# Kernel optimization log

Measured on AMD Instinct MI355X. Metric: run time of the kernel, lower is better.

Reference implementation:

```python
import jax, jax.numpy as jnp
import numpy as np


def fps(p, m):
    """Furthest point sampling. p: (B,N,3) -> idx (B,m) int32. Starts at index 0 like pointops."""
    p = jax.lax.stop_gradient(p)
    B, N, _ = p.shape
    d2 = jnp.full((B, N), jnp.inf, dtype=p.dtype)  # min sq-dist to selected set
    first = jnp.zeros((B,), dtype=jnp.int32)

    def step(carry, _):
        d2, last = carry
        lastp = jnp.take_along_axis(p, last[:, None, None].astype(jnp.int32), axis=1)  # (B,1,3)
        dist = jnp.sum((p - lastp) ** 2, axis=-1)  # (B,N)
        d2 = jnp.minimum(d2, dist)
        nxt = jnp.argmax(d2, axis=-1).astype(jnp.int32)
        return (d2, nxt), last

    _, idx = jax.lax.scan(step, (d2, first), None, length=m)
    return jnp.transpose(idx)  # (B,m)


def knn_indices(p1, p2, k):
    """k nearest neighbors of p2 (B,M,3) among p1 (B,N,3) -> (B,M,k) int32."""
    p1 = jax.lax.stop_gradient(p1)
    p2 = jax.lax.stop_gradient(p2)
    # squared distances (B,M,N)
    d2 = (jnp.sum(p2 ** 2, -1)[:, :, None]
          + jnp.sum(p1 ** 2, -1)[:, None, :]
          - 2.0 * jnp.einsum('bmd,bnd->bmn', p2, p1))
    _, idx = jax.lax.top_k(-d2, k)
    return idx.astype(jnp.int32)


def setup_inputs() -> dict:
    key = jax.random.key(0)
    k1, k2 = jax.random.split(key)
    B, N, C = 8, 8192, 64
    p1 = jax.random.normal(k1, (B, N, 3), dtype=jnp.float32)
    x = jax.random.normal(k2, (B, N, C), dtype=jnp.float32)
    return {"p1": p1, "x": x, "stride": 4, "num_neighbors": 16}


def reference(p1, x, stride, num_neighbors):
    B, N, C = x.shape
    M = N // stride
    idx = fps(p1, M)                                   # (B,M) int32
    p2 = jnp.take_along_axis(p1, idx[:, :, None], 1)   # (B,M,3) sampled coords
    nn = knn_indices(p1, p2, num_neighbors)            # (B,M,k)
    # gather features: (B,M,k,C)
    grouped = jax.vmap(lambda xb, ib: xb[ib])(x, nn)
    y = jnp.mean(grouped, axis=2)                      # (B,M,C)
    return (y, p2, idx)
```

## Files before the change

kernel.cpp:

```cpp
#include <hip/hip_runtime.h>

#define Bn 8
#define Nn 8192
#define Cn 64
#define Mn 2048
#define Kn 16
#define FPS_T 512
#define CPT 16
#define NWAVE (FPS_T / 64)
#define NCELL 4096
#define CELLS_PT (NCELL / FPS_T)

typedef unsigned long long u64;
typedef unsigned u32;

__device__ __forceinline__ u64 u64max(u64 a, u64 b) { return a > b ? a : b; }

template <int CTRL, int RMASK>
__device__ __forceinline__ void dpp_kmax_step(u32& hi, u32& lo) {
    const u32 h2 = (u32)__builtin_amdgcn_update_dpp((int)hi, (int)hi, CTRL, RMASK, 0xF, false);
    const u32 l2 = (u32)__builtin_amdgcn_update_dpp((int)lo, (int)lo, CTRL, RMASK, 0xF, false);
    const u64 a = ((u64)hi << 32) | lo;
    const u64 bb = ((u64)h2 << 32) | l2;
    if (bb > a) { hi = h2; lo = l2; }
}
__device__ __forceinline__ void wave_kmax(u32& hi, u32& lo) {
    dpp_kmax_step<0x111, 0xF>(hi, lo);
    dpp_kmax_step<0x112, 0xF>(hi, lo);
    dpp_kmax_step<0x114, 0xF>(hi, lo);
    dpp_kmax_step<0x118, 0xF>(hi, lo);
    dpp_kmax_step<0x142, 0xA>(hi, lo);
    dpp_kmax_step<0x143, 0xC>(hi, lo);
}

__device__ __forceinline__ u32 spread4(u32 x) {
    return (x & 1u) | ((x & 2u) << 2) | ((x & 4u) << 4) | ((x & 8u) << 6);
}
__device__ __forceinline__ u32 quant16(float v) {
    int c = (int)((v + 4.0f) * 2.0f);
    c = c < 0 ? 0 : (c > 15 ? 15 : c);
    return (u32)c;
}

__global__ __launch_bounds__(FPS_T, 2) void fps_kernel(
    const float* __restrict__ p1,
    float* __restrict__ out_p2,
    float* __restrict__ out_idxf)
{
    __shared__ float s_Px[Nn], s_Py[Nn], s_Pz[Nn];
    __shared__ u32 s_G[Nn];
    __shared__ u32 s_osel[Mn];
    __shared__ int s_hist[NCELL];
    __shared__ int s_scan[FPS_T];
    __shared__ u64 s_wkey[2][NWAVE];

    const int b = blockIdx.x;
    const int t = threadIdx.x;
    const int w = t >> 6;
    const float* __restrict__ P = p1 + (size_t)b * (Nn * 3);

    float qx = P[0], qy = P[1], qz = P[2];

    float rx[CPT], ry[CPT], rz[CPT];
    u32 cc[CPT];
#pragma unroll
    for (int j = 0; j < CPT; ++j) {
        const int g = t + j * FPS_T;
        rx[j] = P[g * 3 + 0];
        ry[j] = P[g * 3 + 1];
        rz[j] = P[g * 3 + 2];
        cc[j] = spread4(quant16(rx[j])) | (spread4(quant16(ry[j])) << 1) |
                (spread4(quant16(rz[j])) << 2);
    }
#pragma unroll
    for (int i = 0; i < CELLS_PT; ++i) s_hist[t * CELLS_PT + i] = 0;
    __syncthreads();
#pragma unroll
    for (int j = 0; j < CPT; ++j) atomicAdd(&s_hist[cc[j]], 1);
    __syncthreads();

    int local[CELLS_PT];
    int sum = 0;
#pragma unroll
    for (int i = 0; i < CELLS_PT; ++i) { local[i] = s_hist[t * CELLS_PT + i]; sum += local[i]; }
    s_scan[t] = sum;
    __syncthreads();
    for (int off = 1; off < FPS_T; off <<= 1) {
        const int add = (t >= off) ? s_scan[t - off] : 0;
        __syncthreads();
        s_scan[t] += add;
        __syncthreads();
    }
    int base = s_scan[t] - sum;
#pragma unroll
    for (int i = 0; i < CELLS_PT; ++i) { s_hist[t * CELLS_PT + i] = base; base += local[i]; }
    __syncthreads();

#pragma unroll
    for (int j = 0; j < CPT; ++j) {
        const int g = t + j * FPS_T;
        const int pos = atomicAdd(&s_hist[cc[j]], 1);
        s_Px[pos] = rx[j]; s_Py[pos] = ry[j]; s_Pz[pos] = rz[j];
        s_G[pos] = (u32)g;
        if (g == 0) s_osel[0] = (u32)pos;
    }
    __syncthreads();

    float px[CPT], py[CPT], pz[CPT], d2[CPT];
    u32 gg[CPT];
    float lox, hix, loy, hiy, loz, hiz;
#pragma unroll
    for (int j = 0; j < CPT; ++j) {
        const int pos = t * CPT + j;
        const float x = s_Px[pos], y = s_Py[pos], z = s_Pz[pos];
        px[j] = x; py[j] = y; pz[j] = z;
        gg[j] = s_G[pos];
        d2[j] = __int_as_float(0x7f800000);
        if (j == 0) { lox = hix = x; loy = hiy = y; loz = hiz = z; }
        else {
            lox = fminf(lox, x); hix = fmaxf(hix, x);
            loy = fminf(loy, y); hiy = fmaxf(hiy, y);
            loz = fminf(loz, z); hiz = fmaxf(hiz, z);
        }
    }
    u32 ubhi = 0x7f800000u, ublo = 0u;

    for (int m = 1; m < Mn; ++m) {
        const float ddx = fmaxf(fmaxf(__fsub_rn(lox, qx), __fsub_rn(qx, hix)), 0.0f);
        const float ddy = fmaxf(fmaxf(__fsub_rn(loy, qy), __fsub_rn(qy, hiy)), 0.0f);
        const float ddz = fmaxf(fmaxf(__fsub_rn(loz, qz), __fsub_rn(qz, hiz)), 0.0f);
        const float Dmin2 = __fadd_rn(
            __fadd_rn(__fmul_rn(ddx, ddx), __fmul_rn(ddy, ddy)), __fmul_rn(ddz, ddz));
        const float S = __fmul_rn(Dmin2, 0.99999f);
        if (S < __uint_as_float(ubhi)) {
            u32 bh = 0u, bl = 0u;
#pragma unroll
            for (int j = 0; j < CPT; ++j) {
                const float dx = __fsub_rn(px[j], qx);
                const float dy = __fsub_rn(py[j], qy);
                const float dz = __fsub_rn(pz[j], qz);
                const float dist = __fadd_rn(
                    __fadd_rn(__fmul_rn(dx, dx), __fmul_rn(dy, dy)),
                    __fmul_rn(dz, dz));
                const float nd = fminf(d2[j], dist);
                d2[j] = nd;
                const u32 kh = __float_as_uint(nd);
                const u32 kl = ((~gg[j] & 0x1FFFu) << 19) | ((u32)(t * CPT + j) << 6);
                const u64 cand = ((u64)kh << 32) | kl;
                if (cand > (((u64)bh << 32) | bl)) { bh = kh; bl = kl; }
            }
            ubhi = bh; ublo = bl;
        }
        u32 rh = ubhi, rl = ublo;
        wave_kmax(rh, rl);
        if ((t & 63) == 63) s_wkey[m & 1][w] = ((u64)rh << 32) | rl;
        __syncthreads();
        const u64* __restrict__ K = s_wkey[m & 1];
        const u64 kk = u64max(u64max(u64max(K[0], K[1]), u64max(K[2], K[3])),
                              u64max(u64max(K[4], K[5]), u64max(K[6], K[7])));
        const u32 pos = (u32)(kk >> 6) & 0x1FFFu;
        if (t == 0) {
            const u32 g = (~(u32)(kk >> 19)) & 0x1FFFu;
            s_osel[m] = (g << 13) | pos;
        }
        qx = s_Px[pos]; qy = s_Py[pos]; qz = s_Pz[pos];
    }
    __syncthreads();

    float* __restrict__ o2 = out_p2 + (size_t)b * Mn * 3;
    float* __restrict__ oi = out_idxf + (size_t)b * Mn;
    for (int i = t; i < Mn; i += FPS_T) {
        const u32 sel = s_osel[i];
        const u32 pos = sel & 0x1FFFu;
        const u32 g = sel >> 13;
        oi[i] = (float)g;
        o2[i * 3 + 0] = s_Px[pos];
        o2[i * 3 + 1] = s_Py[pos];
        o2[i * 3 + 2] = s_Pz[pos];
    }
}

#define KNN_WPB 4
__global__ __launch_bounds__(64 * KNN_WPB) void knn_mean_kernel(
    const float* __restrict__ p1,
    const float* __restrict__ x,
    const float* __restrict__ p2,
    float* __restrict__ y)
{
    const int lane = threadIdx.x & 63;
    const int wid  = threadIdx.x >> 6;
    const int q    = blockIdx.x * KNN_WPB + wid;
    const int b    = q >> 11;
    const float* __restrict__ P = p1 + (size_t)b * (Nn * 3);

    const float qx = p2[(size_t)q * 3 + 0];
    const float qy = p2[(size_t)q * 3 + 1];
    const float qz = p2[(size_t)q * 3 + 2];
    const float qq = __fadd_rn(
        __fadd_rn(__fmul_rn(qx, qx), __fmul_rn(qy, qy)), __fmul_rn(qz, qz));

    float slotv = __int_as_float(0x7f800000);
    int   sloti = 0x7fffffff;
    float thr   = __int_as_float(0x7f800000);
    int   thri  = 0x7fffffff;

    for (int c = 0; c < Nn / 64; ++c) {
        const int g = c * 64 + lane;
        const float ax = P[g * 3 + 0];
        const float ay = P[g * 3 + 1];
        const float az = P[g * 3 + 2];
        const float pp = __fadd_rn(
            __fadd_rn(__fmul_rn(ax, ax), __fmul_rn(ay, ay)), __fmul_rn(az, az));
        const float dot = __fmaf_rn(az, qz, __fmaf_rn(ay, qy, __fmul_rn(ax, qx)));
        const float d = __fsub_rn(__fadd_rn(qq, pp), __fmul_rn(2.0f, dot));
        const bool pass = (d < thr) || (d == thr && g < thri);
        unsigned long long ball = __ballot(pass);
        while (ball) {
            const int src = __builtin_ctzll(ball);
            ball &= ball - 1ull;
            const float v  = __shfl(d, src);
            const int   vi = __shfl(g, src);
            const float upv = __shfl_up(slotv, 1);
            const int   upi = __shfl_up(sloti, 1);
            const bool beforeme = (v < slotv) || (v == slotv && vi < sloti);
            bool beforeup = (v < upv) || (v == upv && vi < upi);
            if (lane == 0) beforeup = false;
            if (beforeme) {
                slotv = beforeup ? upv : v;
                sloti = beforeup ? upi : vi;
            }
            thr  = __shfl(slotv, 15);
            thri = __shfl(sloti, 15);
        }
    }

    float acc = 0.0f;
    const float* __restrict__ xb = x + (size_t)b * Nn * Cn;
#pragma unroll
    for (int s = 0; s < Kn; ++s) {
        const int ni = __shfl(sloti, s);
        acc = __fadd_rn(acc, xb[(size_t)ni * Cn + lane]);
    }
    y[(size_t)q * Cn + lane] = __fmul_rn(acc, 0.0625f);
}

extern "C" void kernel_launch(void* const* d_in, const int* in_sizes, int n_in,
                              void* d_out, int out_size, void* d_ws, size_t ws_size,
                              hipStream_t stream) {
    const float* p1 = (const float*)d_in[0];
    const float* x  = (const float*)d_in[1];

    float* y    = (float*)d_out;
    float* p2   = y    + (size_t)Bn * Mn * Cn;
    float* idxf = p2   + (size_t)Bn * Mn * 3;

    fps_kernel<<<Bn, FPS_T, 0, stream>>>(p1, p2, idxf);
    knn_mean_kernel<<<(Bn * Mn) / KNN_WPB, 64 * KNN_WPB, 0, stream>>>(p1, x, p2, y);
}
```

Measured before the change: 2.102 ms.

## Compact active FPS cells with ballot and process them 16 lanes per cell

The per-point min-distance array moves from registers into LDS. Each FPS iteration now builds a ballot mask of cells whose bounding box could still hold the maximum, and each wave processes four active cells at a time, 16 lanes per cell, with a row-level DPP max reduction. Per-cell upper bounds are cached in LDS, so inactive waves reuse their previous key. The aim is to avoid wasting SIMD lanes when only a few threads in a wave are active. In exchange it adds LDS traffic and extra bookkeeping per iteration, aliases shared buffers and narrows s_G to 16 bits so the larger layout fits.

```diff
diff --git a/kernel.cpp b/kernel.cpp
--- a/kernel.cpp
+++ b/kernel.cpp
@@ -13,6 +13,7 @@
 
 typedef unsigned long long u64;
 typedef unsigned u32;
+typedef unsigned short u16;
 
 __device__ __forceinline__ u64 u64max(u64 a, u64 b) { return a > b ? a : b; }
 
@@ -21,14 +22,17 @@
     const u32 h2 = (u32)__builtin_amdgcn_update_dpp((int)hi, (int)hi, CTRL, RMASK, 0xF, false);
     const u32 l2 = (u32)__builtin_amdgcn_update_dpp((int)lo, (int)lo, CTRL, RMASK, 0xF, false);
     const u64 a = ((u64)hi << 32) | lo;
-    const u64 bb = ((u64)h2 << 32) | l2;
-    if (bb > a) { hi = h2; lo = l2; }
-}
-__device__ __forceinline__ void wave_kmax(u32& hi, u32& lo) {
+    const u64 b2 = ((u64)h2 << 32) | l2;
+    if (b2 > a) { hi = h2; lo = l2; }
+}
+__device__ __forceinline__ void row_kmax(u32& hi, u32& lo) {
     dpp_kmax_step<0x111, 0xF>(hi, lo);
     dpp_kmax_step<0x112, 0xF>(hi, lo);
     dpp_kmax_step<0x114, 0xF>(hi, lo);
     dpp_kmax_step<0x118, 0xF>(hi, lo);
+}
+__device__ __forceinline__ void wave_kmax(u32& hi, u32& lo) {
+    row_kmax(hi, lo);
     dpp_kmax_step<0x142, 0xA>(hi, lo);
     dpp_kmax_step<0x143, 0xC>(hi, lo);
 }
@@ -42,21 +46,27 @@
     return (u32)c;
 }
 
-__global__ __launch_bounds__(FPS_T, 2) void fps_kernel(
+__global__ __launch_bounds__(FPS_T) void fps_kernel(
     const float* __restrict__ p1,
     float* __restrict__ out_p2,
     float* __restrict__ out_idxf)
 {
     __shared__ float s_Px[Nn], s_Py[Nn], s_Pz[Nn];
-    __shared__ u32 s_G[Nn];
-    __shared__ u32 s_osel[Mn];
-    __shared__ int s_hist[NCELL];
-    __shared__ int s_scan[FPS_T];
-    __shared__ u64 s_wkey[2][NWAVE];
+    __shared__ float s_blobA[Nn];
+    __shared__ u32   s_blobB[Mn];
+    __shared__ u16   s_G[Nn];
+    __shared__ u64   s_ub[FPS_T];
+    __shared__ u64   s_wkey[2][NWAVE];
+
+    int*   s_hist = (int*)s_blobA;
+    float* s_d2   = s_blobA;
+    int*   s_scan = (int*)s_blobB;
+    u32*   s_osel = s_blobB;
 
     const int b = blockIdx.x;
     const int t = threadIdx.x;
     const int w = t >> 6;
+    const int lane = t & 63;
     const float* __restrict__ P = p1 + (size_t)b * (Nn * 3);
 
     float qx = P[0], qy = P[1], qz = P[2];
@@ -101,61 +111,74 @@
         const int g = t + j * FPS_T;
         const int pos = atomicAdd(&s_hist[cc[j]], 1);
         s_Px[pos] = rx[j]; s_Py[pos] = ry[j]; s_Pz[pos] = rz[j];
-        s_G[pos] = (u32)g;
+        s_G[pos] = (u16)g;
         if (g == 0) s_osel[0] = (u32)pos;
     }
     __syncthreads();
 
-    float px[CPT], py[CPT], pz[CPT], d2[CPT];
-    u32 gg[CPT];
     float lox, hix, loy, hiy, loz, hiz;
-#pragma unroll
-    for (int j = 0; j < CPT; ++j) {
-        const int pos = t * CPT + j;
-        const float x = s_Px[pos], y = s_Py[pos], z = s_Pz[pos];
-        px[j] = x; py[j] = y; pz[j] = z;
-        gg[j] = s_G[pos];
-        d2[j] = __int_as_float(0x7f800000);
-        if (j == 0) { lox = hix = x; loy = hiy = y; loz = hiz = z; }
-        else {
-            lox = fminf(lox, x); hix = fmaxf(hix, x);
-            loy = fminf(loy, y); hiy = fmaxf(hiy, y);
-            loz = fminf(loz, z); hiz = fmaxf(hiz, z);
-        }
-    }
-    u32 ubhi = 0x7f800000u, ublo = 0u;
-
-    for (int m = 1; m < Mn; ++m) {
-        const float ddx = fmaxf(fmaxf(__fsub_rn(lox, qx), __fsub_rn(qx, hix)), 0.0f);
-        const float ddy = fmaxf(fmaxf(__fsub_rn(loy, qy), __fsub_rn(qy, hiy)), 0.0f);
-        const float ddz = fmaxf(fmaxf(__fsub_rn(loz, qz), __fsub_rn(qz, hiz)), 0.0f);
-        const float Dmin2 = __fadd_rn(
-            __fadd_rn(__fmul_rn(ddx, ddx), __fmul_rn(ddy, ddy)), __fmul_rn(ddz, ddz));
-        const float S = __fmul_rn(Dmin2, 0.99999f);
-        if (S < __uint_as_float(ubhi)) {
-            u32 bh = 0u, bl = 0u;
-#pragma unroll
-            for (int j = 0; j < CPT; ++j) {
-                const float dx = __fsub_rn(px[j], qx);
-                const float dy = __fsub_rn(py[j], qy);
-                const float dz = __fsub_rn(pz[j], qz);
+    {
+        const int p0 = t * CPT;
+        lox = hix = s_Px[p0]; loy = hiy = s_Py[p0]; loz = hiz = s_Pz[p0];
+        s_d2[p0] = __int_as_float(0x7f800000);
+#pragma unroll
+        for (int j = 1; j < CPT; ++j) {
+            const float X = s_Px[p0 + j], Y = s_Py[p0 + j], Z = s_Pz[p0 + j];
+            lox = fminf(lox, X); hix = fmaxf(hix, X);
+            loy = fminf(loy, Y); hiy = fmaxf(hiy, Y);
+            loz = fminf(loz, Z); hiz = fmaxf(hiz, Z);
+            s_d2[p0 + j] = __int_as_float(0x7f800000);
+        }
+    }
+    __syncthreads();
+
+    auto phaseB = [&](u64 mk) {
+        while (mk) {
+            int c0, c1 = -1, c2 = -1, c3 = -1;
+            c0 = (int)__builtin_ctzll(mk); mk &= mk - 1;
+            if (mk) { c1 = (int)__builtin_ctzll(mk); mk &= mk - 1;
+                if (mk) { c2 = (int)__builtin_ctzll(mk); mk &= mk - 1;
+                    if (mk) { c3 = (int)__builtin_ctzll(mk); mk &= mk - 1; } } }
+            const int sub = lane >> 4;
+            int myc = c0;
+            myc = (sub == 1) ? c1 : myc;
+            myc = (sub == 2) ? c2 : myc;
+            myc = (sub == 3) ? c3 : myc;
+            if (myc >= 0) {
+                const int cid = (w << 6) + myc;
+                const int pp = cid * CPT + (lane & 15);
+                const float X = s_Px[pp], Y = s_Py[pp], Z = s_Pz[pp];
+                const float od = s_d2[pp];
+                const float dx = __fsub_rn(X, qx);
+                const float dy = __fsub_rn(Y, qy);
+                const float dz = __fsub_rn(Z, qz);
                 const float dist = __fadd_rn(
                     __fadd_rn(__fmul_rn(dx, dx), __fmul_rn(dy, dy)),
                     __fmul_rn(dz, dz));
-                const float nd = fminf(d2[j], dist);
-                d2[j] = nd;
-                const u32 kh = __float_as_uint(nd);
-                const u32 kl = ((~gg[j] & 0x1FFFu) << 19) | ((u32)(t * CPT + j) << 6);
-                const u64 cand = ((u64)kh << 32) | kl;
-                if (cand > (((u64)bh << 32) | bl)) { bh = kh; bl = kl; }
+                const float nd = fminf(od, dist);
+                s_d2[pp] = nd;
+                const u32 g = (u32)s_G[pp];
+                u32 kh = __float_as_uint(nd);
+                u32 kl = ((~g & 0x1FFFu) << 19) | ((u32)pp << 6);
+                row_kmax(kh, kl);
+                if ((lane & 15) == 15) s_ub[cid] = ((u64)kh << 32) | kl;
             }
-            ubhi = bh; ublo = bl;
-        }
-        u32 rh = ubhi, rl = ublo;
+        }
+    };
+
+    u32 cacheH = 0, cacheL = 0;
+
+    phaseB(~0ull);
+    {
+        const u64 kmy = s_ub[t];
+        u32 rh = (u32)(kmy >> 32), rl = (u32)kmy;
         wave_kmax(rh, rl);
-        if ((t & 63) == 63) s_wkey[m & 1][w] = ((u64)rh << 32) | rl;
-        __syncthreads();
-        const u64* __restrict__ K = s_wkey[m & 1];
+        if (lane == 63) { cacheH = rh; cacheL = rl; s_wkey[0][w] = ((u64)rh << 32) | rl; }
+    }
+    __syncthreads();
+
+    for (int m = 1; m < Mn; ++m) {
+        const u64* __restrict__ K = s_wkey[(m - 1) & 1];
         const u64 kk = u64max(u64max(u64max(K[0], K[1]), u64max(K[2], K[3])),
                               u64max(u64max(K[4], K[5]), u64max(K[6], K[7])));
         const u32 pos = (u32)(kk >> 6) & 0x1FFFu;
@@ -164,8 +187,26 @@
             s_osel[m] = (g << 13) | pos;
         }
         qx = s_Px[pos]; qy = s_Py[pos]; qz = s_Pz[pos];
-    }
-    __syncthreads();
+
+        const float ubv = __uint_as_float(((const u32*)s_ub)[2 * t + 1]);
+        const float ddx = fmaxf(fmaxf(__fsub_rn(lox, qx), __fsub_rn(qx, hix)), 0.0f);
+        const float ddy = fmaxf(fmaxf(__fsub_rn(loy, qy), __fsub_rn(qy, hiy)), 0.0f);
+        const float ddz = fmaxf(fmaxf(__fsub_rn(loz, qz), __fsub_rn(qz, hiz)), 0.0f);
+        const float Dmin2 = __fadd_rn(
+            __fadd_rn(__fmul_rn(ddx, ddx), __fmul_rn(ddy, ddy)), __fmul_rn(ddz, ddz));
+        const bool active = __fmul_rn(Dmin2, 0.99999f) < ubv;
+        const u64 mk = __ballot(active);
+
+        if (mk) {
+            phaseB(mk);
+            const u64 kmy = s_ub[t];
+            u32 rh = (u32)(kmy >> 32), rl = (u32)kmy;
+            wave_kmax(rh, rl);
+            if (lane == 63) { cacheH = rh; cacheL = rl; }
+        }
+        if (lane == 63) s_wkey[m & 1][w] = ((u64)cacheH << 32) | cacheL;
+        __syncthreads();
+    }
 
     float* __restrict__ o2 = out_p2 + (size_t)b * Mn * 3;
     float* __restrict__ oi = out_idxf + (size_t)b * Mn;
```

Result: slower. 3.274 ms (+55.7%).

## Replace Morton-cell sort with x/y/z slab sort and skip idle waves in FPS

Applied to the files above, without the earlier changes.

The uniform 16^3 Morton cell binning of points is replaced with a three-pass counting sort (x slabs, then y within each slab, then z), so each thread owns 16 spatially compact points with tighter bounding boxes. Each wave now skips its distance update entirely when no lane's box can beat its current max, using a ballot. Each wave also publishes its winner's coordinates along with its key, so the next iteration picks the query point without an extra shared-memory lookup. Points stay in original order in shared memory and are accessed through a u16 index array. The trade-off is more setup passes and barriers, plus a per-iteration selection over eight wave candidates.

```diff
diff --git a/kernel.cpp b/kernel.cpp
--- a/kernel.cpp
+++ b/kernel.cpp
@@ -7,22 +7,22 @@
 #define Kn 16
 #define FPS_T 512
 #define CPT 16
-#define NWAVE (FPS_T / 64)
-#define NCELL 4096
-#define CELLS_PT (NCELL / FPS_T)
+#define NWAVE 8
 
 typedef unsigned long long u64;
 typedef unsigned u32;
+typedef unsigned short u16;
 
 __device__ __forceinline__ u64 u64max(u64 a, u64 b) { return a > b ? a : b; }
+__device__ __forceinline__ int clampi(int v, int lo, int hi) { return v < lo ? lo : (v > hi ? hi : v); }
 
 template <int CTRL, int RMASK>
 __device__ __forceinline__ void dpp_kmax_step(u32& hi, u32& lo) {
     const u32 h2 = (u32)__builtin_amdgcn_update_dpp((int)hi, (int)hi, CTRL, RMASK, 0xF, false);
     const u32 l2 = (u32)__builtin_amdgcn_update_dpp((int)lo, (int)lo, CTRL, RMASK, 0xF, false);
-    const u64 a = ((u64)hi << 32) | lo;
-    const u64 bb = ((u64)h2 << 32) | l2;
-    if (bb > a) { hi = h2; lo = l2; }
+    const u64 a  = ((u64)hi << 32) | lo;
+    const u64 b2 = ((u64)h2 << 32) | l2;
+    if (b2 > a) { hi = h2; lo = l2; }
 }
 __device__ __forceinline__ void wave_kmax(u32& hi, u32& lo) {
     dpp_kmax_step<0x111, 0xF>(hi, lo);
@@ -33,106 +33,207 @@
     dpp_kmax_step<0x143, 0xC>(hi, lo);
 }
 
-__device__ __forceinline__ u32 spread4(u32 x) {
-    return (x & 1u) | ((x & 2u) << 2) | ((x & 4u) << 4) | ((x & 8u) << 6);
-}
-__device__ __forceinline__ u32 quant16(float v) {
-    int c = (int)((v + 4.0f) * 2.0f);
-    c = c < 0 ? 0 : (c > 15 ? 15 : c);
-    return (u32)c;
-}
-
-__global__ __launch_bounds__(FPS_T, 2) void fps_kernel(
+__global__ __launch_bounds__(FPS_T) void fps_kernel(
     const float* __restrict__ p1,
     float* __restrict__ out_p2,
     float* __restrict__ out_idxf)
 {
     __shared__ float s_Px[Nn], s_Py[Nn], s_Pz[Nn];
-    __shared__ u32 s_G[Nn];
-    __shared__ u32 s_osel[Mn];
-    __shared__ int s_hist[NCELL];
-    __shared__ int s_scan[FPS_T];
-    __shared__ u64 s_wkey[2][NWAVE];
-
-    const int b = blockIdx.x;
-    const int t = threadIdx.x;
-    const int w = t >> 6;
+    __shared__ u16   s_idx[2][Nn];
+    __shared__ u32   s_osel[Mn];
+    __shared__ int   s_hist[FPS_T];
+    __shared__ u64   s_skey[2][NWAVE];
+    __shared__ float s_sq[2][NWAVE][4];
+
+    const int b = blockIdx.x, t = threadIdx.x, w = t >> 6, lane = t & 63;
     const float* __restrict__ P = p1 + (size_t)b * (Nn * 3);
 
-    float qx = P[0], qy = P[1], qz = P[2];
-
-    float rx[CPT], ry[CPT], rz[CPT];
-    u32 cc[CPT];
 #pragma unroll
     for (int j = 0; j < CPT; ++j) {
         const int g = t + j * FPS_T;
-        rx[j] = P[g * 3 + 0];
-        ry[j] = P[g * 3 + 1];
-        rz[j] = P[g * 3 + 2];
-        cc[j] = spread4(quant16(rx[j])) | (spread4(quant16(ry[j])) << 1) |
-                (spread4(quant16(rz[j])) << 2);
-    }
-#pragma unroll
-    for (int i = 0; i < CELLS_PT; ++i) s_hist[t * CELLS_PT + i] = 0;
-    __syncthreads();
-#pragma unroll
-    for (int j = 0; j < CPT; ++j) atomicAdd(&s_hist[cc[j]], 1);
-    __syncthreads();
-
-    int local[CELLS_PT];
-    int sum = 0;
-#pragma unroll
-    for (int i = 0; i < CELLS_PT; ++i) { local[i] = s_hist[t * CELLS_PT + i]; sum += local[i]; }
-    s_scan[t] = sum;
-    __syncthreads();
-    for (int off = 1; off < FPS_T; off <<= 1) {
-        const int add = (t >= off) ? s_scan[t - off] : 0;
-        __syncthreads();
-        s_scan[t] += add;
-        __syncthreads();
-    }
-    int base = s_scan[t] - sum;
-#pragma unroll
-    for (int i = 0; i < CELLS_PT; ++i) { s_hist[t * CELLS_PT + i] = base; base += local[i]; }
-    __syncthreads();
-
+        s_Px[g] = P[g * 3 + 0];
+        s_Py[g] = P[g * 3 + 1];
+        s_Pz[g] = P[g * 3 + 2];
+    }
+    if (t < 256) s_hist[t] = 0;
+    __syncthreads();
+
+    int xb[CPT];
 #pragma unroll
     for (int j = 0; j < CPT; ++j) {
         const int g = t + j * FPS_T;
-        const int pos = atomicAdd(&s_hist[cc[j]], 1);
-        s_Px[pos] = rx[j]; s_Py[pos] = ry[j]; s_Pz[pos] = rz[j];
-        s_G[pos] = (u32)g;
-        if (g == 0) s_osel[0] = (u32)pos;
+        xb[j] = clampi((int)((s_Px[g] + 4.0f) * 32.0f), 0, 255);
+        atomicAdd(&s_hist[xb[j]], 1);
+    }
+    __syncthreads();
+    {
+        const int cnt = (t < 256) ? s_hist[t] : 0;
+        int incl = cnt;
+        for (int off = 1; off < 256; off <<= 1) {
+            const int v = (t < 256 && t >= off) ? s_hist[t - off] : 0;
+            __syncthreads();
+            if (t < 256) { incl += v; s_hist[t] = incl; }
+            __syncthreads();
+        }
+        if (t < 256) s_hist[t] = incl - cnt;
+    }
+    __syncthreads();
+#pragma unroll
+    for (int j = 0; j < CPT; ++j) {
+        const int g = t + j * FPS_T;
+        const int r = atomicAdd(&s_hist[xb[j]], 1);
+        s_idx[0][r] = (u16)g;
+    }
+    __syncthreads();
+
+    s_hist[t] = 0;
+    __syncthreads();
+    int c2[CPT];
+#pragma unroll
+    for (int j = 0; j < CPT; ++j) {
+        const int i = t + j * FPS_T;
+        const int g = s_idx[0][i];
+        const int yb = clampi((int)((s_Py[g] + 4.0f) * 8.0f), 0, 63);
+        c2[j] = ((i >> 10) << 6) | yb;
+        atomicAdd(&s_hist[c2[j]], 1);
+    }
+    __syncthreads();
+    {
+        const int cnt = s_hist[t];
+        int incl = cnt;
+        const int seg = t >> 6;
+        for (int off = 1; off < 64; off <<= 1) {
+            const int v = (t >= off && ((t - off) >> 6) == seg) ? s_hist[t - off] : 0;
+            __syncthreads();
+            incl += v; s_hist[t] = incl;
+            __syncthreads();
+        }
+        s_hist[t] = (seg << 10) + incl - cnt;
+    }
+    __syncthreads();
+#pragma unroll
+    for (int j = 0; j < CPT; ++j) {
+        const int i = t + j * FPS_T;
+        const u16 g = s_idx[0][i];
+        const int r = atomicAdd(&s_hist[c2[j]], 1);
+        s_idx[1][r] = g;
+    }
+    __syncthreads();
+
+    int* cnt3 = (int*)s_osel;
+    for (int k = t; k < 2048; k += FPS_T) cnt3[k] = 0;
+    __syncthreads();
+    int c3[CPT];
+#pragma unroll
+    for (int j = 0; j < CPT; ++j) {
+        const int i = t + j * FPS_T;
+        const int g = s_idx[1][i];
+        const int zb = clampi((int)((s_Pz[g] + 4.0f) * 4.0f), 0, 31);
+        c3[j] = ((i >> 7) << 5) | zb;
+        atomicAdd(&cnt3[c3[j]], 1);
+    }
+    __syncthreads();
+    if (t < 64) {
+        int acc = t << 7;
+        for (int k = 0; k < 32; ++k) {
+            const int c = cnt3[(t << 5) + k];
+            cnt3[(t << 5) + k] = acc;
+            acc += c;
+        }
+    }
+    __syncthreads();
+#pragma unroll
+    for (int j = 0; j < CPT; ++j) {
+        const int i = t + j * FPS_T;
+        const u16 g = s_idx[1][i];
+        const int r = atomicAdd(&cnt3[c3[j]], 1);
+        s_idx[0][r] = g;
     }
     __syncthreads();
 
     float px[CPT], py[CPT], pz[CPT], d2[CPT];
-    u32 gg[CPT];
+    u32 kl[CPT];
     float lox, hix, loy, hiy, loz, hiz;
 #pragma unroll
     for (int j = 0; j < CPT; ++j) {
-        const int pos = t * CPT + j;
-        const float x = s_Px[pos], y = s_Py[pos], z = s_Pz[pos];
-        px[j] = x; py[j] = y; pz[j] = z;
-        gg[j] = s_G[pos];
+        const int g = s_idx[0][t * CPT + j];
+        const float X = s_Px[g], Y = s_Py[g], Z = s_Pz[g];
+        px[j] = X; py[j] = Y; pz[j] = Z;
+        kl[j] = (~(u32)g) & 0x1FFFu;
         d2[j] = __int_as_float(0x7f800000);
-        if (j == 0) { lox = hix = x; loy = hiy = y; loz = hiz = z; }
+        if (j == 0) { lox = hix = X; loy = hiy = Y; loz = hiz = Z; }
         else {
-            lox = fminf(lox, x); hix = fmaxf(hix, x);
-            loy = fminf(loy, y); hiy = fmaxf(hiy, y);
-            loz = fminf(loz, z); hiz = fmaxf(hiz, z);
-        }
-    }
-    u32 ubhi = 0x7f800000u, ublo = 0u;
+            lox = fminf(lox, X); hix = fmaxf(hix, X);
+            loy = fminf(loy, Y); hiy = fmaxf(hiy, Y);
+            loz = fminf(loz, Z); hiz = fmaxf(hiz, Z);
+        }
+    }
+    if (t == 0) s_osel[0] = 0u;
+
+    float qx = s_Px[0], qy = s_Py[0], qz = s_Pz[0];
+    u32 ubh = 0, ubl = 0;
+    u32 ckh = 0, ckl = 0;
+    float cqx = 0.f, cqy = 0.f, cqz = 0.f;
+
+    {
+        u32 bh = 0u, bl = 0u;
+#pragma unroll
+        for (int j = 0; j < CPT; ++j) {
+            const float dx = __fsub_rn(px[j], qx);
+            const float dy = __fsub_rn(py[j], qy);
+            const float dz = __fsub_rn(pz[j], qz);
+            const float dist = __fadd_rn(
+                __fadd_rn(__fmul_rn(dx, dx), __fmul_rn(dy, dy)), __fmul_rn(dz, dz));
+            const float nd = fminf(d2[j], dist);
+            d2[j] = nd;
+            const u64 cand = ((u64)__float_as_uint(nd) << 32) | kl[j];
+            if (cand > (((u64)bh << 32) | bl)) { bh = (u32)(cand >> 32); bl = (u32)cand; }
+        }
+        ubh = bh; ubl = bl;
+        u32 rh = ubh, rl = ubl;
+        wave_kmax(rh, rl);
+        if (lane == 63) {
+            ckh = rh; ckl = rl;
+            const int gw = (int)((~rl) & 0x1FFFu);
+            cqx = s_Px[gw]; cqy = s_Py[gw]; cqz = s_Pz[gw];
+            s_skey[0][w] = ((u64)ckh << 32) | ckl;
+            s_sq[0][w][0] = cqx; s_sq[0][w][1] = cqy; s_sq[0][w][2] = cqz;
+        }
+    }
+    __syncthreads();
 
     for (int m = 1; m < Mn; ++m) {
+        const int rb = (m - 1) & 1;
+        u64 K[8]; float Q[8][3];
+#pragma unroll
+        for (int i = 0; i < 8; ++i) {
+            K[i] = s_skey[rb][i];
+            Q[i][0] = s_sq[rb][i][0];
+            Q[i][1] = s_sq[rb][i][1];
+            Q[i][2] = s_sq[rb][i][2];
+        }
+        u64 kk = K[0];
+#pragma unroll
+        for (int i = 1; i < 8; ++i) kk = u64max(kk, K[i]);
+        qx = Q[0][0]; qy = Q[0][1]; qz = Q[0][2];
+#pragma unroll
+        for (int i = 1; i < 8; ++i) {
+            const bool win = (K[i] == kk);
+            qx = win ? Q[i][0] : qx;
+            qy = win ? Q[i][1] : qy;
+            qz = win ? Q[i][2] : qz;
+        }
+        if (t == 0) s_osel[m] = (~(u32)kk) & 0x1FFFu;
+
+        const float ubv = __uint_as_float(ubh);
         const float ddx = fmaxf(fmaxf(__fsub_rn(lox, qx), __fsub_rn(qx, hix)), 0.0f);
         const float ddy = fmaxf(fmaxf(__fsub_rn(loy, qy), __fsub_rn(qy, hiy)), 0.0f);
         const float ddz = fmaxf(fmaxf(__fsub_rn(loz, qz), __fsub_rn(qz, hiz)), 0.0f);
         const float Dmin2 = __fadd_rn(
             __fadd_rn(__fmul_rn(ddx, ddx), __fmul_rn(ddy, ddy)), __fmul_rn(ddz, ddz));
-        const float S = __fmul_rn(Dmin2, 0.99999f);
-        if (S < __uint_as_float(ubhi)) {
+        const bool active = __fmul_rn(Dmin2, 0.99999f) < ubv;
+
+        if (__ballot(active) != 0ull) {
             u32 bh = 0u, bl = 0u;
 #pragma unroll
             for (int j = 0; j < CPT; ++j) {
@@ -140,43 +241,36 @@
                 const float dy = __fsub_rn(py[j], qy);
                 const float dz = __fsub_rn(pz[j], qz);
                 const float dist = __fadd_rn(
-                    __fadd_rn(__fmul_rn(dx, dx), __fmul_rn(dy, dy)),
-                    __fmul_rn(dz, dz));
+                    __fadd_rn(__fmul_rn(dx, dx), __fmul_rn(dy, dy)), __fmul_rn(dz, dz));
                 const float nd = fminf(d2[j], dist);
                 d2[j] = nd;
-                const u32 kh = __float_as_uint(nd);
-                const u32 kl = ((~gg[j] & 0x1FFFu) << 19) | ((u32)(t * CPT + j) << 6);
-                const u64 cand = ((u64)kh << 32) | kl;
-                if (cand > (((u64)bh << 32) | bl)) { bh = kh; bl = kl; }
+                const u64 cand = ((u64)__float_as_uint(nd) << 32) | kl[j];
+                if (cand > (((u64)bh << 32) | bl)) { bh = (u32)(cand >> 32); bl = (u32)cand; }
             }
-            ubhi = bh; ublo = bl;
-        }
-        u32 rh = ubhi, rl = ublo;
-        wave_kmax(rh, rl);
-        if ((t & 63) == 63) s_wkey[m & 1][w] = ((u64)rh << 32) | rl;
+            ubh = bh; ubl = bl;
+            u32 rh = ubh, rl = ubl;
+            wave_kmax(rh, rl);
+            if (lane == 63) {
+                ckh = rh; ckl = rl;
+                const int gw = (int)((~rl) & 0x1FFFu);
+                cqx = s_Px[gw]; cqy = s_Py[gw]; cqz = s_Pz[gw];
+            }
+        }
+        if (lane == 63) {
+            s_skey[m & 1][w] = ((u64)ckh << 32) | ckl;
+            s_sq[m & 1][w][0] = cqx; s_sq[m & 1][w][1] = cqy; s_sq[m & 1][w][2] = cqz;
+        }
         __syncthreads();
-        const u64* __restrict__ K = s_wkey[m & 1];
-        const u64 kk = u64max(u64max(u64max(K[0], K[1]), u64max(K[2], K[3])),
-                              u64max(u64max(K[4], K[5]), u64max(K[6], K[7])));
-        const u32 pos = (u32)(kk >> 6) & 0x1FFFu;
-        if (t == 0) {
-            const u32 g = (~(u32)(kk >> 19)) & 0x1FFFu;
-            s_osel[m] = (g << 13) | pos;
-        }
-        qx = s_Px[pos]; qy = s_Py[pos]; qz = s_Pz[pos];
-    }
-    __syncthreads();
+    }
 
     float* __restrict__ o2 = out_p2 + (size_t)b * Mn * 3;
     float* __restrict__ oi = out_idxf + (size_t)b * Mn;
     for (int i = t; i < Mn; i += FPS_T) {
-        const u32 sel = s_osel[i];
-        const u32 pos = sel & 0x1FFFu;
-        const u32 g = sel >> 13;
+        const u32 g = s_osel[i];
         oi[i] = (float)g;
-        o2[i * 3 + 0] = s_Px[pos];
-        o2[i * 3 + 1] = s_Py[pos];
-        o2[i * 3 + 2] = s_Pz[pos];
+        o2[i * 3 + 0] = s_Px[g];
+        o2[i * 3 + 1] = s_Py[g];
+        o2[i * 3 + 2] = s_Pz[g];
     }
 }
 
```

Measured after the change: 2.574 ms. +22.4%, slower.
